# Kernel optimization log

Measured on AMD Instinct MI355X. Metric: run time of the kernel, lower is better.

Reference implementation:

```python
import jax, jax.numpy as jnp
import numpy as np

N0, N1, N2 = 300000, 60000, 6000
E1, E2 = 1200000, 300000
R, D_IN, D_H, D_OUT = 4, 128, 128, 64
HBUF = 30000
BN_EPS = 1e-5


def setup_inputs() -> dict:
    key = jax.random.key(0)
    ks = jax.random.split(key, 16)
    inp = {
        "x": jax.random.normal(ks[0], (N0, D_IN), jnp.float32),
        "src1": jax.random.randint(ks[1], (E1,), 0, N0, jnp.int32),
        "dst1": jax.random.randint(ks[2], (E1,), 0, N1, jnp.int32),
        "et1": jax.random.randint(ks[3], (E1,), 0, R, jnp.int32),
        "src2": jax.random.randint(ks[4], (E2,), 0, N1, jnp.int32),
        "dst2": jax.random.randint(ks[5], (E2,), 0, N2, jnp.int32),
        "et2": jax.random.randint(ks[6], (E2,), 0, R, jnp.int32),
        # history_map values in [-1, HBUF-1); -1 means "no cached history"
        "history_map": jax.random.randint(ks[7], (N1,), 0, HBUF, jnp.int32) - 1,
        "history_buffer": jax.random.normal(ks[8], (HBUF, D_H), jnp.float32),
        "W1": jax.random.normal(ks[9], (R, D_IN, D_H), jnp.float32) / np.sqrt(D_IN),
        "Wself1": jax.random.normal(ks[10], (D_IN, D_H), jnp.float32) / np.sqrt(D_IN),
        "b1": jnp.zeros((D_H,), jnp.float32),
        "gamma": jnp.ones((D_H,), jnp.float32),
        "beta": jnp.zeros((D_H,), jnp.float32),
        "W2": jax.random.normal(ks[11], (R, D_H, D_OUT), jnp.float32) / np.sqrt(D_H),
        "Wself2": jax.random.normal(ks[12], (D_H, D_OUT), jnp.float32) / np.sqrt(D_H),
        "b2": jnp.zeros((D_OUT,), jnp.float32),
    }
    return inp


def relgraphconv(x, src, dst, et, n_out, W, Wself, b):
    # per-relation transform of all src nodes: [R, N, out]
    xW = jnp.einsum('ni,rio->rno', x, W)
    msg = xW[et, src]                                   # [E, out] gather
    agg = jax.ops.segment_sum(msg, dst, num_segments=n_out)  # scatter-add
    # DGL block: dst nodes are the first n_out src nodes (self loop)
    return agg + x[:n_out] @ Wself + b


def reference(x, src1, dst1, et1, src2, dst2, et2, history_map,
              history_buffer, W1, Wself1, b1, gamma, beta, W2, Wself2, b2):
    # layer 1: RGCN + history overwrite
    h = relgraphconv(x, src1, dst1, et1, N1, W1, Wself1, b1)
    valid = history_map >= 0
    safe_idx = jnp.where(valid, history_map, 0)
    h = jnp.where(valid[:, None], history_buffer[safe_idx], h)
    # BatchNorm1d (training: batch statistics), relu; dropout p=0.0
    mean = jnp.mean(h, axis=0)
    var = jnp.var(h, axis=0)
    h = (h - mean) * jax.lax.rsqrt(var + BN_EPS) * gamma + beta
    h = jax.nn.relu(h)
    # layer 2: RGCN (history_size=0 path), log-softmax
    out = relgraphconv(h, src2, dst2, et2, N2, W2, Wself2, b2)
    return jax.nn.log_softmax(out, axis=-1)
```

## Files before the change

### kernel.cpp

```cpp
#include <hip/hip_runtime.h>
#include <hip/hip_bf16.h>

#define N0 300000
#define N1 60000
#define N2 6000
#define E1 1200000
#define E2 300000
#define D 128
#define DO 64
#define HBUF 30000

#define WL_CAP 32768
#define UC_CAP 256
#define CAP 192

#define CONV_BLKS 1875
#define NSCAN_BLKS 235
#define ESCAN_BLKS 4688

typedef __attribute__((ext_vector_type(8))) short bfrag8;
typedef __attribute__((ext_vector_type(4))) float f32x4;

__device__ __forceinline__ float bf2f(unsigned int u) {
    union { unsigned int i; float f; } c; c.i = u << 16; return c.f;
}
__device__ __forceinline__ unsigned short f2bf(float f) {
    return __bfloat16_as_ushort(__float2bfloat16(f));
}

__global__ void k_zero(float* __restrict__ hfix, int* __restrict__ mcount,
                       int* __restrict__ degcnt, int* __restrict__ cnt,
                       int* __restrict__ nuc) {
    int i = blockIdx.x * 256 + threadIdx.x;
    int stride = gridDim.x * 256;
    for (int j = i; j < UC_CAP * D; j += stride) hfix[j] = 0.f;
    for (int j = i; j < HBUF; j += stride) mcount[j] = 0;
    for (int j = i; j < N2; j += stride) degcnt[j] = 0;
    if (i == 0) { *cnt = 0; *nuc = 0; }
}

__global__ void __launch_bounds__(256) k_A(
        const float* __restrict__ hist, unsigned short* __restrict__ histbf,
        const int* __restrict__ hmap, int* __restrict__ mcount,
        int* __restrict__ nuc, int* __restrict__ uc_slot, int* __restrict__ uc_node,
        const int* __restrict__ dst1, int* __restrict__ cnt, int* __restrict__ list,
        const int* __restrict__ src2, const int* __restrict__ dst2,
        const int* __restrict__ et2, int* __restrict__ degcnt,
        int* __restrict__ epay) {
    int b = blockIdx.x, tid = threadIdx.x;
    if (b < CONV_BLKS) {
        int i = b * 256 + tid;
        const float4* h4 = (const float4*)hist;
        float4 u = h4[(size_t)i * 2], v = h4[(size_t)i * 2 + 1];
        union { unsigned short s[8]; uint4 q; } o;
        o.s[0] = f2bf(u.x); o.s[1] = f2bf(u.y); o.s[2] = f2bf(u.z); o.s[3] = f2bf(u.w);
        o.s[4] = f2bf(v.x); o.s[5] = f2bf(v.y); o.s[6] = f2bf(v.z); o.s[7] = f2bf(v.w);
        *(uint4*)(histbf + (size_t)i * 8) = o.q;
    } else if (b < CONV_BLKS + NSCAN_BLKS) {
        int node = (b - CONV_BLKS) * 256 + tid;
        if (node < N1) {
            int m = hmap[node];
            if (m >= 0) {
                atomicAdd(&mcount[m], 1);
            } else {
                int slot = atomicAdd(nuc, 1);
                if (slot < UC_CAP) { uc_slot[node] = slot; uc_node[slot] = node; }
            }
        }
    } else {
        int e = (b - CONV_BLKS - NSCAN_BLKS) * 256 + tid;
        if (e < E2) {
            int d = dst2[e];
            int pos = atomicAdd(&degcnt[d], 1);
            if (pos < CAP) epay[d * CAP + pos] = src2[e] | (et2[e] << 16);
        }
        if (e < E1 && hmap[dst1[e]] < 0) {
            int i = atomicAdd(cnt, 1);
            if (i < WL_CAP) list[i] = e;
        }
    }
}

__global__ void __launch_bounds__(256) k_wl2(
        const float* __restrict__ x, const int* __restrict__ src1,
        const int* __restrict__ dst1, const int* __restrict__ et1,
        const float* __restrict__ W1, const float* __restrict__ Wself1,
        const float* __restrict__ b1, const int* __restrict__ cnt,
        const int* __restrict__ list, const int* __restrict__ uc_slot,
        const int* __restrict__ uc_node, const int* __restrict__ nuc,
        const int* __restrict__ hmap, int* __restrict__ remap,
        const float* __restrict__ hist, const int* __restrict__ mcount,
        float* __restrict__ hfix, float* __restrict__ psum) {
    __shared__ float ls1[256], ls2[256];
    int b = blockIdx.x, tid = threadIdx.x;
    if (b < 16) {
        int c = tid & 127, half = tid >> 7;
        int n = *cnt; if (n > WL_CAP) n = WL_CAP;
        for (int i = b * 2 + half; i < n; i += 32) {
            int e = list[i];
            int s = src1[e], d = dst1[e], t = et1[e];
            int slot = uc_slot[d];
            if (slot < 0 || slot >= UC_CAP) continue;
            float acc = 0.f;
            for (int k = 0; k < D; k++) acc += x[(size_t)s * D + k] * W1[(t * D + k) * D + c];
            atomicAdd(&hfix[slot * D + c], acc);
        }
    } else if (b < 24) {
        int n = *nuc; if (n > UC_CAP) n = UC_CAP;
        int c = tid & 127, half = tid >> 7;
        for (int slot = (b - 16) * 2 + half; slot < n; slot += 16) {
            int node = uc_node[slot];
            float acc = b1[c];
            for (int k = 0; k < D; k++) acc += x[(size_t)node * D + k] * Wself1[k * D + c];
            atomicAdd(&hfix[slot * D + c], acc);
        }
    } else if (b < 259) {
        int node = (b - 24) * 256 + tid;
        if (node < N1) {
            int m = hmap[node];
            if (m >= 0) {
                remap[node] = m;
            } else {
                int s = uc_slot[node];
                if (s < 0) s = 0;
                if (s > UC_CAP - 1) s = UC_CAP - 1;
                remap[node] = HBUF + s;
            }
        }
    } else {
        int bs = b - 259;
        int c = tid & 127, half = tid >> 7;
        float S = 0.f, SS = 0.f;
        for (int r = bs * 2 + half; r < HBUF; r += 512) {
            float w = (float)mcount[r];
            if (w == 0.f) continue;
            float v = hist[(size_t)r * D + c];
            S += w * v; SS += w * v * v;
        }
        ls1[tid] = S; ls2[tid] = SS;
        __syncthreads();
        if (tid < 128) {
            psum[bs * 256 + tid] = ls1[tid] + ls1[tid + 128];
            psum[bs * 256 + 128 + tid] = ls2[tid] + ls2[tid + 128];
        }
    }
}

__global__ void k_mid(const float* __restrict__ psum, const float* __restrict__ hfix,
                      const int* __restrict__ nuc,
                      const float* __restrict__ gamma, const float* __restrict__ beta,
                      float* __restrict__ params,
                      unsigned short* __restrict__ histbf,
                      const float* __restrict__ W2, const float* __restrict__ Wself2,
                      unsigned short* __restrict__ BF) {
    int b = blockIdx.x, tid = threadIdx.x;
    if (b == 0) {
        if (tid < 128) {
            float S = 0.f, SS = 0.f;
            for (int r = 0; r < 256; r++) {
                S += psum[r * 256 + tid];
                SS += psum[r * 256 + 128 + tid];
            }
            int n = *nuc; if (n > UC_CAP) n = UC_CAP;
            for (int slot = 0; slot < n; slot++) {
                float v = hfix[slot * D + tid];
                S += v; SS += v * v;
            }
            float mean = S / (float)N1;
            float var = SS / (float)N1 - mean * mean;
            float sc = gamma[tid] * rsqrtf(var + 1e-5f);
            params[tid] = sc;
            params[128 + tid] = beta[tid] - mean * sc;
        }
    } else if (b == 1) {
        for (int i = tid; i < UC_CAP * D; i += 256)
            histbf[(size_t)HBUF * D + i] = f2bf(hfix[i]);
    } else {
        int idx = (b - 2) * 256 + tid;
        int j = idx & 7, lane = (idx >> 3) & 63, sub = (idx >> 9) & 15, g = idx >> 13;
        int kt = sub >> 2, ct = sub & 3;
        int k = kt * 32 + (lane >> 4) * 8 + j;
        int col = ct * 16 + (lane & 15);
        float v = (g < 4) ? W2[(g * D + k) * DO + col] : Wself2[k * DO + col];
        BF[idx] = f2bf(v);
    }
}

#define AGG_ACC(P, V) { \
    int t_ = (P) >> 16; \
    float f0_ = fmaxf(bf2f((V) & 0xffff) * sc0 + sh0, 0.f); \
    float f1_ = fmaxf(bf2f((V) >> 16) * sc1 + sh1, 0.f); \
    acc[0][0] += (t_ == 0) ? f0_ : 0.f; acc[0][1] += (t_ == 0) ? f1_ : 0.f; \
    acc[1][0] += (t_ == 1) ? f0_ : 0.f; acc[1][1] += (t_ == 1) ? f1_ : 0.f; \
    acc[2][0] += (t_ == 2) ? f0_ : 0.f; acc[2][1] += (t_ == 2) ? f1_ : 0.f; \
    acc[3][0] += (t_ == 3) ? f0_ : 0.f; acc[3][1] += (t_ == 3) ? f1_ : 0.f; }

__global__ void __launch_bounds__(256) k_agg(const unsigned int* __restrict__ hbu,
                                             const int* __restrict__ remap,
                                             const int* __restrict__ degcnt,
                                             const int* __restrict__ epay,
                                             const float* __restrict__ params,
                                             unsigned int* __restrict__ aggbu) {
    __shared__ float red[4 * 4 * 128];
    int d = blockIdx.x;
    int wave = threadIdx.x >> 6, lane = threadIdx.x & 63;
    float sc0 = params[2 * lane],     sh0 = params[128 + 2 * lane];
    float sc1 = params[2 * lane + 1], sh1 = params[128 + 2 * lane + 1];
    float acc[4][2] = {};
    int j1 = degcnt[d]; if (j1 > CAP) j1 = CAP;
    const int* ep = epay + d * CAP;
    int j = wave;
    for (; j + 12 < j1; j += 16) {
        int p0 = ep[j], p1 = ep[j + 4], p2 = ep[j + 8], p3 = ep[j + 12];
        int r0 = remap[p0 & 0xffff], r1 = remap[p1 & 0xffff];
        int r2 = remap[p2 & 0xffff], r3 = remap[p3 & 0xffff];
        unsigned int v0 = hbu[(size_t)r0 * 64 + lane];
        unsigned int v1 = hbu[(size_t)r1 * 64 + lane];
        unsigned int v2 = hbu[(size_t)r2 * 64 + lane];
        unsigned int v3 = hbu[(size_t)r3 * 64 + lane];
        AGG_ACC(p0, v0); AGG_ACC(p1, v1); AGG_ACC(p2, v2); AGG_ACC(p3, v3);
    }
    for (; j < j1; j += 4) {
        int p = ep[j];
        unsigned int v = hbu[(size_t)remap[p & 0xffff] * 64 + lane];
        AGG_ACC(p, v);
    }
#pragma unroll
    for (int t = 0; t < 4; t++) {
        red[(wave * 4 + t) * 128 + 2 * lane]     = acc[t][0];
        red[(wave * 4 + t) * 128 + 2 * lane + 1] = acc[t][1];
    }
    __syncthreads();
    int t = threadIdx.x >> 6, l2 = threadIdx.x & 63;
    float s0 = 0.f, s1 = 0.f;
#pragma unroll
    for (int w = 0; w < 4; w++) {
        s0 += red[(w * 4 + t) * 128 + 2 * l2];
        s1 += red[(w * 4 + t) * 128 + 2 * l2 + 1];
    }
    aggbu[((size_t)t * N2 + d) * 64 + l2] =
        (unsigned int)f2bf(s0) | ((unsigned int)f2bf(s1) << 16);
}

__global__ void __launch_bounds__(256) k_gemm2(const unsigned short* __restrict__ aggb,
                                               const unsigned short* __restrict__ histbf,
                                               const int* __restrict__ remap,
                                               const unsigned short* __restrict__ BF,
                                               const float* __restrict__ params,
                                               const float* __restrict__ b2,
                                               float* __restrict__ out) {
    int row0 = blockIdx.x * 64;
    int wave = threadIdx.x >> 6, lane = threadIdx.x & 63;
    int r = row0 + wave * 16 + (lane & 15);
    int rl = (r < N2) ? r : N2 - 1;
    int ridx = remap[rl];
    int kb = (lane >> 4) * 8;
    f32x4 acc[4] = {};
#pragma unroll
    for (int kt = 0; kt < 4; kt++) {
#pragma unroll
        for (int g = 0; g < 5; g++) {
            bfrag8 a;
            if (g < 4) {
                a = *reinterpret_cast<const bfrag8*>(aggb + ((size_t)(g * N2 + rl) * D + kt * 32 + kb));
            } else {
                bfrag8 raw = *reinterpret_cast<const bfrag8*>(histbf + ((size_t)ridx * D + kt * 32 + kb));
#pragma unroll
                for (int j = 0; j < 8; j++) {
                    int c = kt * 32 + kb + j;
                    float f = bf2f((unsigned int)(unsigned short)raw[j]);
                    f = fmaxf(f * params[c] + params[128 + c], 0.f);
                    a[j] = (short)f2bf(f);
                }
            }
#pragma unroll
            for (int ct = 0; ct < 4; ct++) {
                bfrag8 bb = *reinterpret_cast<const bfrag8*>(BF + ((((g * 4 + kt) * 4 + ct) * 64 + lane) * 8));
                acc[ct] = __builtin_amdgcn_mfma_f32_16x16x32_bf16(a, bb, acc[ct], 0, 0, 0);
            }
        }
    }
    float bb4[4];
#pragma unroll
    for (int ct = 0; ct < 4; ct++) bb4[ct] = b2[ct * 16 + (lane & 15)];
    int srow = row0 + wave * 16 + (lane >> 4) * 4;
#pragma unroll
    for (int i = 0; i < 4; i++) {
        float v[4];
#pragma unroll
        for (int ct = 0; ct < 4; ct++) v[ct] = acc[ct][i] + bb4[ct];
        float m = fmaxf(fmaxf(v[0], v[1]), fmaxf(v[2], v[3]));
#pragma unroll
        for (int sh = 1; sh <= 8; sh <<= 1) m = fmaxf(m, __shfl_xor(m, sh, 64));
        float s = 0.f;
#pragma unroll
        for (int ct = 0; ct < 4; ct++) s += expf(v[ct] - m);
#pragma unroll
        for (int sh = 1; sh <= 8; sh <<= 1) s += __shfl_xor(s, sh, 64);
        float lg = m + logf(s);
        int rr = srow + i;
        if (rr < N2) {
#pragma unroll
            for (int ct = 0; ct < 4; ct++)
                out[(size_t)rr * DO + ct * 16 + (lane & 15)] = v[ct] - lg;
        }
    }
}

extern "C" void kernel_launch(void* const* d_in, const int* in_sizes, int n_in,
                              void* d_out, int out_size, void* d_ws, size_t ws_size,
                              hipStream_t stream) {
    const float* x      = (const float*)d_in[0];
    const int* src1     = (const int*)d_in[1];
    const int* dst1     = (const int*)d_in[2];
    const int* et1      = (const int*)d_in[3];
    const int* src2     = (const int*)d_in[4];
    const int* dst2     = (const int*)d_in[5];
    const int* et2      = (const int*)d_in[6];
    const int* hmap     = (const int*)d_in[7];
    const float* hist   = (const float*)d_in[8];
    const float* W1     = (const float*)d_in[9];
    const float* Wself1 = (const float*)d_in[10];
    const float* b1     = (const float*)d_in[11];
    const float* gamma  = (const float*)d_in[12];
    const float* beta   = (const float*)d_in[13];
    const float* W2     = (const float*)d_in[14];
    const float* Wself2 = (const float*)d_in[15];
    const float* b2     = (const float*)d_in[16];
    float* out = (float*)d_out;

    char* ws = (char*)d_ws;
    unsigned short* histbf = (unsigned short*)(ws);
    unsigned short* aggb   = (unsigned short*)(ws + 7745536);
    unsigned short* BF     = (unsigned short*)(ws + 13889536);
    float* hfix            = (float*)(ws + 13971456);
    int* uc_node           = (int*)(ws + 14102528);
    int* uc_slot           = (int*)(ws + 14103552);
    int* remap             = (int*)(ws + 14343552);
    int* epay              = (int*)(ws + 14583552);
    int* mcount            = (int*)(ws + 19191552);
    int* degcnt            = (int*)(ws + 19311552);
    float* psum            = (float*)(ws + 19335552);
    int* list              = (int*)(ws + 19597696);
    float* params          = (float*)(ws + 19728768);
    int* cnt               = (int*)(ws + 19729792);
    int* nuc               = (int*)(ws + 19729796);

    k_zero<<<128, 256, 0, stream>>>(hfix, mcount, degcnt, cnt, nuc);
    k_A<<<CONV_BLKS + NSCAN_BLKS + ESCAN_BLKS, 256, 0, stream>>>(
        hist, histbf, hmap, mcount, nuc, uc_slot, uc_node,
        dst1, cnt, list, src2, dst2, et2, degcnt, epay);
    k_wl2<<<515, 256, 0, stream>>>(x, src1, dst1, et1, W1, Wself1, b1,
                                   cnt, list, uc_slot, uc_node, nuc,
                                   hmap, remap, hist, mcount, hfix, psum);
    k_mid<<<162, 256, 0, stream>>>(psum, hfix, nuc, gamma, beta, params,
                                   histbf, W2, Wself2, BF);
    k_agg<<<N2, 256, 0, stream>>>((const unsigned int*)histbf, remap, degcnt,
                                  epay, params, (unsigned int*)aggb);
    k_gemm2<<<94, 256, 0, stream>>>(aggb, histbf, remap, BF, params, b2, out);
}
```

Measured before the change: 114.6 us.

## Transform unique history rows before aggregation instead of aggregating then GEMM

Layer 2 is reordered to transform-then-aggregate. All 30256 unique source rows (history buffer plus uncached fixes) are first multiplied by the 4 relation weights and the self weight into a bf16 Y table of 320 columns. The per-destination aggregation then gathers 64-wide bf16 rows indexed by relation, and the bias, self loop and log-softmax are fused into that kernel. This removes the separate agg buffer and GEMM kernel and shrinks the gathered data per edge, but adds a GEMM over 30k rows and a roughly 19 MB intermediate write. It also pads degcnt counters to 16-int stride to reduce atomic contention.

```diff
diff --git a/kernel.cpp b/kernel.cpp
--- a/kernel.cpp
+++ b/kernel.cpp
@@ -9,6 +9,7 @@
 #define D 128
 #define DO 64
 #define HBUF 30000
+#define NROWS (HBUF + UC_CAP)
 
 #define WL_CAP 32768
 #define UC_CAP 256
@@ -35,7 +36,7 @@
     int stride = gridDim.x * 256;
     for (int j = i; j < UC_CAP * D; j += stride) hfix[j] = 0.f;
     for (int j = i; j < HBUF; j += stride) mcount[j] = 0;
-    for (int j = i; j < N2; j += stride) degcnt[j] = 0;
+    for (int j = i; j < N2 * 16; j += stride) degcnt[j] = 0;
     if (i == 0) { *cnt = 0; *nuc = 0; }
 }
 
@@ -71,7 +72,7 @@
         int e = (b - CONV_BLKS - NSCAN_BLKS) * 256 + tid;
         if (e < E2) {
             int d = dst2[e];
-            int pos = atomicAdd(&degcnt[d], 1);
+            int pos = atomicAdd(&degcnt[d * 16], 1);
             if (pos < CAP) epay[d * CAP + pos] = src2[e] | (et2[e] << 16);
         }
         if (e < E1 && hmap[dst1[e]] < 0) {
@@ -186,124 +187,94 @@
     }
 }
 
-#define AGG_ACC(P, V) { \
-    int t_ = (P) >> 16; \
-    float f0_ = fmaxf(bf2f((V) & 0xffff) * sc0 + sh0, 0.f); \
-    float f1_ = fmaxf(bf2f((V) >> 16) * sc1 + sh1, 0.f); \
-    acc[0][0] += (t_ == 0) ? f0_ : 0.f; acc[0][1] += (t_ == 0) ? f1_ : 0.f; \
-    acc[1][0] += (t_ == 1) ? f0_ : 0.f; acc[1][1] += (t_ == 1) ? f1_ : 0.f; \
-    acc[2][0] += (t_ == 2) ? f0_ : 0.f; acc[2][1] += (t_ == 2) ? f1_ : 0.f; \
-    acc[3][0] += (t_ == 3) ? f0_ : 0.f; acc[3][1] += (t_ == 3) ? f1_ : 0.f; }
-
-__global__ void __launch_bounds__(256) k_agg(const unsigned int* __restrict__ hbu,
-                                             const int* __restrict__ remap,
-                                             const int* __restrict__ degcnt,
-                                             const int* __restrict__ epay,
-                                             const float* __restrict__ params,
-                                             unsigned int* __restrict__ aggbu) {
-    __shared__ float red[4 * 4 * 128];
+__global__ void __launch_bounds__(256) k_trans(
+        const unsigned short* __restrict__ histbf,
+        const unsigned short* __restrict__ BF,
+        const float* __restrict__ params,
+        unsigned short* __restrict__ Y) {
+    int row0 = blockIdx.x * 64;
+    int wave = threadIdx.x >> 6, lane = threadIdx.x & 63;
+    int r = row0 + wave * 16 + (lane & 15);
+    int rl = (r < NROWS) ? r : NROWS - 1;
+    int kb = (lane >> 4) * 8;
+    f32x4 acc[5][4] = {};
+#pragma unroll
+    for (int kt = 0; kt < 4; kt++) {
+        bfrag8 raw = *reinterpret_cast<const bfrag8*>(histbf + (size_t)rl * D + kt * 32 + kb);
+        bfrag8 a;
+#pragma unroll
+        for (int j = 0; j < 8; j++) {
+            int c = kt * 32 + kb + j;
+            float f = bf2f((unsigned int)(unsigned short)raw[j]);
+            f = fmaxf(f * params[c] + params[128 + c], 0.f);
+            a[j] = (short)f2bf(f);
+        }
+#pragma unroll
+        for (int g = 0; g < 5; g++) {
+#pragma unroll
+            for (int ct = 0; ct < 4; ct++) {
+                bfrag8 bb = *reinterpret_cast<const bfrag8*>(BF + ((((g * 4 + kt) * 4 + ct) * 64 + lane) * 8));
+                acc[g][ct] = __builtin_amdgcn_mfma_f32_16x16x32_bf16(a, bb, acc[g][ct], 0, 0, 0);
+            }
+        }
+    }
+    int srow = row0 + wave * 16 + (lane >> 4) * 4;
+    int col = lane & 15;
+#pragma unroll
+    for (int g = 0; g < 5; g++) {
+#pragma unroll
+        for (int ct = 0; ct < 4; ct++) {
+#pragma unroll
+            for (int i = 0; i < 4; i++) {
+                int rr = srow + i;
+                if (rr < NROWS)
+                    Y[(size_t)rr * 320 + g * 64 + ct * 16 + col] = f2bf(acc[g][ct][i]);
+            }
+        }
+    }
+}
+
+__global__ void __launch_bounds__(256) k_agg2(const unsigned short* __restrict__ Y,
+                                              const int* __restrict__ remap,
+                                              const int* __restrict__ degcnt,
+                                              const int* __restrict__ epay,
+                                              const float* __restrict__ b2,
+                                              float* __restrict__ out) {
+    __shared__ float red[4][64];
     int d = blockIdx.x;
-    int wave = threadIdx.x >> 6, lane = threadIdx.x & 63;
-    float sc0 = params[2 * lane],     sh0 = params[128 + 2 * lane];
-    float sc1 = params[2 * lane + 1], sh1 = params[128 + 2 * lane + 1];
-    float acc[4][2] = {};
-    int j1 = degcnt[d]; if (j1 > CAP) j1 = CAP;
+    int wave = threadIdx.x >> 6, o = threadIdx.x & 63;
+    float acc = 0.f;
+    int j1 = degcnt[d * 16]; if (j1 > CAP) j1 = CAP;
     const int* ep = epay + d * CAP;
     int j = wave;
     for (; j + 12 < j1; j += 16) {
         int p0 = ep[j], p1 = ep[j + 4], p2 = ep[j + 8], p3 = ep[j + 12];
         int r0 = remap[p0 & 0xffff], r1 = remap[p1 & 0xffff];
         int r2 = remap[p2 & 0xffff], r3 = remap[p3 & 0xffff];
-        unsigned int v0 = hbu[(size_t)r0 * 64 + lane];
-        unsigned int v1 = hbu[(size_t)r1 * 64 + lane];
-        unsigned int v2 = hbu[(size_t)r2 * 64 + lane];
-        unsigned int v3 = hbu[(size_t)r3 * 64 + lane];
-        AGG_ACC(p0, v0); AGG_ACC(p1, v1); AGG_ACC(p2, v2); AGG_ACC(p3, v3);
+        unsigned short v0 = Y[(size_t)r0 * 320 + (p0 >> 16) * 64 + o];
+        unsigned short v1 = Y[(size_t)r1 * 320 + (p1 >> 16) * 64 + o];
+        unsigned short v2 = Y[(size_t)r2 * 320 + (p2 >> 16) * 64 + o];
+        unsigned short v3 = Y[(size_t)r3 * 320 + (p3 >> 16) * 64 + o];
+        acc += bf2f(v0) + bf2f(v1) + bf2f(v2) + bf2f(v3);
     }
     for (; j < j1; j += 4) {
         int p = ep[j];
-        unsigned int v = hbu[(size_t)remap[p & 0xffff] * 64 + lane];
-        AGG_ACC(p, v);
-    }
-#pragma unroll
-    for (int t = 0; t < 4; t++) {
-        red[(wave * 4 + t) * 128 + 2 * lane]     = acc[t][0];
-        red[(wave * 4 + t) * 128 + 2 * lane + 1] = acc[t][1];
-    }
+        int rr = remap[p & 0xffff];
+        acc += bf2f((unsigned int)Y[(size_t)rr * 320 + (p >> 16) * 64 + o]);
+    }
+    red[wave][o] = acc;
     __syncthreads();
-    int t = threadIdx.x >> 6, l2 = threadIdx.x & 63;
-    float s0 = 0.f, s1 = 0.f;
-#pragma unroll
-    for (int w = 0; w < 4; w++) {
-        s0 += red[(w * 4 + t) * 128 + 2 * l2];
-        s1 += red[(w * 4 + t) * 128 + 2 * l2 + 1];
-    }
-    aggbu[((size_t)t * N2 + d) * 64 + l2] =
-        (unsigned int)f2bf(s0) | ((unsigned int)f2bf(s1) << 16);
-}
-
-__global__ void __launch_bounds__(256) k_gemm2(const unsigned short* __restrict__ aggb,
-                                               const unsigned short* __restrict__ histbf,
-                                               const int* __restrict__ remap,
-                                               const unsigned short* __restrict__ BF,
-                                               const float* __restrict__ params,
-                                               const float* __restrict__ b2,
-                                               float* __restrict__ out) {
-    int row0 = blockIdx.x * 64;
-    int wave = threadIdx.x >> 6, lane = threadIdx.x & 63;
-    int r = row0 + wave * 16 + (lane & 15);
-    int rl = (r < N2) ? r : N2 - 1;
-    int ridx = remap[rl];
-    int kb = (lane >> 4) * 8;
-    f32x4 acc[4] = {};
-#pragma unroll
-    for (int kt = 0; kt < 4; kt++) {
-#pragma unroll
-        for (int g = 0; g < 5; g++) {
-            bfrag8 a;
-            if (g < 4) {
-                a = *reinterpret_cast<const bfrag8*>(aggb + ((size_t)(g * N2 + rl) * D + kt * 32 + kb));
-            } else {
-                bfrag8 raw = *reinterpret_cast<const bfrag8*>(histbf + ((size_t)ridx * D + kt * 32 + kb));
-#pragma unroll
-                for (int j = 0; j < 8; j++) {
-                    int c = kt * 32 + kb + j;
-                    float f = bf2f((unsigned int)(unsigned short)raw[j]);
-                    f = fmaxf(f * params[c] + params[128 + c], 0.f);
-                    a[j] = (short)f2bf(f);
-                }
-            }
-#pragma unroll
-            for (int ct = 0; ct < 4; ct++) {
-                bfrag8 bb = *reinterpret_cast<const bfrag8*>(BF + ((((g * 4 + kt) * 4 + ct) * 64 + lane) * 8));
-                acc[ct] = __builtin_amdgcn_mfma_f32_16x16x32_bf16(a, bb, acc[ct], 0, 0, 0);
-            }
-        }
-    }
-    float bb4[4];
-#pragma unroll
-    for (int ct = 0; ct < 4; ct++) bb4[ct] = b2[ct * 16 + (lane & 15)];
-    int srow = row0 + wave * 16 + (lane >> 4) * 4;
-#pragma unroll
-    for (int i = 0; i < 4; i++) {
-        float v[4];
-#pragma unroll
-        for (int ct = 0; ct < 4; ct++) v[ct] = acc[ct][i] + bb4[ct];
-        float m = fmaxf(fmaxf(v[0], v[1]), fmaxf(v[2], v[3]));
-#pragma unroll
-        for (int sh = 1; sh <= 8; sh <<= 1) m = fmaxf(m, __shfl_xor(m, sh, 64));
-        float s = 0.f;
-#pragma unroll
-        for (int ct = 0; ct < 4; ct++) s += expf(v[ct] - m);
-#pragma unroll
-        for (int sh = 1; sh <= 8; sh <<= 1) s += __shfl_xor(s, sh, 64);
-        float lg = m + logf(s);
-        int rr = srow + i;
-        if (rr < N2) {
-#pragma unroll
-            for (int ct = 0; ct < 4; ct++)
-                out[(size_t)rr * DO + ct * 16 + (lane & 15)] = v[ct] - lg;
-        }
+    if (wave == 0) {
+        float v = red[0][o] + red[1][o] + red[2][o] + red[3][o] + b2[o]
+                + bf2f((unsigned int)Y[(size_t)remap[d] * 320 + 256 + o]);
+        float m = v;
+#pragma unroll
+        for (int sh = 32; sh; sh >>= 1) m = fmaxf(m, __shfl_xor(m, sh, 64));
+        float ex = expf(v - m);
+        float s = ex;
+#pragma unroll
+        for (int sh = 32; sh; sh >>= 1) s += __shfl_xor(s, sh, 64);
+        out[(size_t)d * DO + o] = v - m - logf(s);
     }
 }
 
@@ -331,20 +302,20 @@
 
     char* ws = (char*)d_ws;
     unsigned short* histbf = (unsigned short*)(ws);
-    unsigned short* aggb   = (unsigned short*)(ws + 7745536);
-    unsigned short* BF     = (unsigned short*)(ws + 13889536);
-    float* hfix            = (float*)(ws + 13971456);
-    int* uc_node           = (int*)(ws + 14102528);
-    int* uc_slot           = (int*)(ws + 14103552);
-    int* remap             = (int*)(ws + 14343552);
-    int* epay              = (int*)(ws + 14583552);
-    int* mcount            = (int*)(ws + 19191552);
-    int* degcnt            = (int*)(ws + 19311552);
-    float* psum            = (float*)(ws + 19335552);
-    int* list              = (int*)(ws + 19597696);
-    float* params          = (float*)(ws + 19728768);
-    int* cnt               = (int*)(ws + 19729792);
-    int* nuc               = (int*)(ws + 19729796);
+    unsigned short* Y      = (unsigned short*)(ws + 7745536);
+    unsigned short* BF     = (unsigned short*)(ws + 27109376);
+    float* hfix            = (float*)(ws + 27191296);
+    int* uc_node           = (int*)(ws + 27322368);
+    int* uc_slot           = (int*)(ws + 27323392);
+    int* remap             = (int*)(ws + 27563392);
+    int* epay              = (int*)(ws + 27803392);
+    int* mcount            = (int*)(ws + 32411392);
+    int* degcnt            = (int*)(ws + 32531392);
+    float* psum            = (float*)(ws + 32915392);
+    int* list              = (int*)(ws + 33177536);
+    float* params          = (float*)(ws + 33308608);
+    int* cnt               = (int*)(ws + 33309632);
+    int* nuc               = (int*)(ws + 33309636);
 
     k_zero<<<128, 256, 0, stream>>>(hfix, mcount, degcnt, cnt, nuc);
     k_A<<<CONV_BLKS + NSCAN_BLKS + ESCAN_BLKS, 256, 0, stream>>>(
@@ -355,7 +326,6 @@
                                    hmap, remap, hist, mcount, hfix, psum);
     k_mid<<<162, 256, 0, stream>>>(psum, hfix, nuc, gamma, beta, params,
                                    histbf, W2, Wself2, BF);
-    k_agg<<<N2, 256, 0, stream>>>((const unsigned int*)histbf, remap, degcnt,
-                                  epay, params, (unsigned int*)aggb);
-    k_gemm2<<<94, 256, 0, stream>>>(aggb, histbf, remap, BF, params, b2, out);
-}
+    k_trans<<<(NROWS + 63) / 64, 256, 0, stream>>>(histbf, BF, params, Y);
+    k_agg2<<<N2, 256, 0, stream>>>(Y, remap, degcnt, epay, b2, out);
+}
```

Measured after the change: 128.1 us. 11.8% more time.
